# Kernel optimization log

Hardware: AMD Instinct MI355X
Metric: run time of the kernel (lower is better)

Reference implementation:

```python
import jax, jax.numpy as jnp
import numpy as np

IDIM = 128
ODIM = 128
G = 8          # deformable groups
KH = KW = 3
K = KH * KW


def conv3x3(x, w, b):
    # x: [B,C,H,W], w: [O,I,3,3], stride 1, pad 1
    y = jax.lax.conv_general_dilated(x, w, (1, 1), ((1, 1), (1, 1)),
                                     dimension_numbers=('NCHW', 'OIHW', 'NCHW'))
    return y + b[None, :, None, None]


def deform_conv_v2(x, offset, mask, w, b):
    # x: [B,C,H,W]; offset: [B,2*G*K,H,W]; mask: [B,G*K,H,W] (pre-sigmoid)
    B, C, H, W = x.shape
    Cg = C // G
    off = offset.reshape(B, G, 2 * K, H, W)
    dy = off[:, :, 0::2]            # [B,G,K,H,W]
    dx = off[:, :, 1::2]
    m = jax.nn.sigmoid(mask).reshape(B, G, K, H, W)

    ky, kx = jnp.meshgrid(jnp.arange(KH), jnp.arange(KW), indexing='ij')
    ky = ky.reshape(K).astype(x.dtype)
    kx = kx.reshape(K).astype(x.dtype)
    hh = jnp.arange(H, dtype=x.dtype)
    ww = jnp.arange(W, dtype=x.dtype)
    # sampling positions (stride 1, pad 1, dilation 1)
    py = dy + (ky[:, None, None] + hh[None, :, None] - 1.0)   # [B,G,K,H,W]
    px = dx + (kx[:, None, None] + ww[None, None, :] - 1.0)

    y0 = jnp.floor(py)
    x0 = jnp.floor(px)
    ly = py - y0
    lx = px - x0

    x_flat = x.reshape(B, G, Cg, H * W)

    def gather(yi, xi):
        valid = ((yi >= 0) & (yi < H) & (xi >= 0) & (xi < W)).astype(x.dtype)
        yc = jnp.clip(yi, 0, H - 1).astype(jnp.int32)
        xc = jnp.clip(xi, 0, W - 1).astype(jnp.int32)
        idx = (yc * W + xc).reshape(B, G, 1, K * H * W)
        v = jnp.take_along_axis(x_flat, jnp.broadcast_to(idx, (B, G, Cg, K * H * W)), axis=3)
        return v.reshape(B, G, Cg, K, H, W) * valid[:, :, None]

    # bilinear interpolation with zero padding, fused with modulation mask
    v = (gather(y0, x0) * ((1 - ly) * (1 - lx))[:, :, None]
         + gather(y0, x0 + 1) * ((1 - ly) * lx)[:, :, None]
         + gather(y0 + 1, x0) * (ly * (1 - lx))[:, :, None]
         + gather(y0 + 1, x0 + 1) * (ly * lx)[:, :, None])
    v = v * m[:, :, None]                                      # [B,G,Cg,K,H,W]

    wr = w.reshape(w.shape[0], G, Cg, K)
    out = jnp.einsum('bgckhw,ogck->bohw', v, wr)
    return out + b[None, :, None, None]


def setup_inputs() -> dict:
    key = jax.random.key(0)
    ks = jax.random.split(key, 12)
    B, H, W = 2, 96, 96
    s = 0.05
    return {
        'R1': jax.random.normal(ks[0], (B, IDIM, H, W), jnp.float32),
        'Q0': jax.random.normal(ks[1], (B, IDIM, H, W), jnp.float32),
        'w1': jax.random.normal(ks[2], (ODIM, IDIM, 3, 3), jnp.float32) * s,
        'b1': jax.random.normal(ks[3], (ODIM,), jnp.float32) * s,
        'w2': jax.random.normal(ks[4], (ODIM, ODIM, 3, 3), jnp.float32) * s,
        'b2': jax.random.normal(ks[5], (ODIM,), jnp.float32) * s,
        'w_om': jax.random.normal(ks[6], (G * 3 * K, ODIM, 3, 3), jnp.float32) * s,
        'b_om': jax.random.normal(ks[7], (G * 3 * K,), jnp.float32) * s,
        'w_dcn': jax.random.normal(ks[8], (ODIM, IDIM, 3, 3), jnp.float32) * s,
        'b_dcn': jax.random.normal(ks[9], (ODIM,), jnp.float32) * s,
        'w_rq': jax.random.normal(ks[10], (ODIM, 2 * ODIM, 3, 3), jnp.float32) * s,
        'b_rq': jax.random.normal(ks[11], (ODIM,), jnp.float32) * s,
    }


def reference(R1, Q0, w1, b1, w2, b2, w_om, b_om, w_dcn, b_dcn, w_rq, b_rq):
    off = jax.nn.relu(conv3x3(R1 - Q0, w1, b1))
    off = jax.nn.relu(conv3x3(off, w2, b2))
    om = conv3x3(off, w_om, b_om)                 # [B, 3*G*K, H, W]
    o1, o2, mask = jnp.split(om, 3, axis=1)
    offset = jnp.concatenate([o1, o2], axis=1)    # [B, 2*G*K, H, W]
    fea = jax.nn.relu(deform_conv_v2(R1, offset, mask, w_dcn, b_dcn))
    fused = jnp.concatenate([fea, Q0], axis=1)
    return jax.nn.relu(conv3x3(fused, w_rq, b_rq))
```

## Files before the change

kernel.cpp:

```cpp
#include <hip/hip_runtime.h>

#define HH 96
#define WW 96
#define HW 9216
#define NPIX 18432
#define OMC 216
#define PP 9604

typedef __attribute__((ext_vector_type(8))) short short8x;
typedef __attribute__((ext_vector_type(8))) unsigned short ushort8x;
typedef __attribute__((ext_vector_type(4))) float f32x4;

__device__ __forceinline__ f32x4 mfma16(short8x a, short8x b, f32x4 c) {
    return __builtin_amdgcn_mfma_f32_16x16x32_bf16(a, b, c, 0, 0, 0);
}
__device__ __forceinline__ unsigned short f2bf(float f) {
    unsigned int u = __float_as_uint(f);
    u = (u + 0x7FFFu + ((u >> 16) & 1u)) >> 16;
    return (unsigned short)u;
}
__device__ __forceinline__ float bf2f(unsigned short b) {
    return __uint_as_float((unsigned int)b << 16);
}
__device__ __forceinline__ void split2(float v, unsigned short& h, unsigned short& l) {
    h = f2bf(v);
    l = f2bf(v - bf2f(h));
}
__device__ __forceinline__ void gld_lds16(const unsigned short* src, unsigned short* dst) {
    __builtin_amdgcn_global_load_lds(
        (const __attribute__((address_space(1))) unsigned int*)src,
        (__attribute__((address_space(3))) unsigned int*)dst, 16, 0, 0);
}

__global__ __launch_bounds__(256) void zero_borders(
    unsigned short* __restrict__ diffb,
    unsigned short* __restrict__ t1,
    unsigned short* __restrict__ catb)
{
    int i = blockIdx.x * 256 + threadIdx.x;
    if (i >= 776) return;
    int b = i / 388, r = i % 388;
    int y, x;
    if      (r < 98)  { y = 0;          x = r; }
    else if (r < 196) { y = 97;         x = r - 98; }
    else if (r < 292) { y = r - 196 + 1; x = 0; }
    else              { y = r - 292 + 1; x = 97; }
    size_t P = (size_t)b * PP + (size_t)y * 98 + x;
    ushort8x z = {};
    #pragma unroll
    for (int c = 0; c < 32; ++c) *(ushort8x*)&diffb[P * 256 + c * 8] = z;
    #pragma unroll
    for (int c = 0; c < 32; ++c) *(ushort8x*)&t1[P * 256 + c * 8] = z;
    #pragma unroll
    for (int c = 0; c < 64; ++c) *(ushort8x*)&catb[P * 512 + c * 8] = z;
}

__global__ __launch_bounds__(256) void prep_acts(
    const float* __restrict__ R1, const float* __restrict__ Q0,
    unsigned short* __restrict__ r1b,
    unsigned short* __restrict__ diffb,
    unsigned short* __restrict__ cat)
{
    __shared__ float tR[128][64];
    __shared__ float tQ[128][64];
    int tid = threadIdx.x;
    int p0  = blockIdx.x * 64;
    int b   = p0 / HW;
    int rem0 = p0 % HW;

    for (int e = tid; e < 2048; e += 256) {
        int c = e >> 4, j = e & 15;
        size_t base = ((size_t)(b * 128 + c)) * HW + rem0;
        *(float4*)&tR[c][j * 4] = *(const float4*)(R1 + base + j * 4);
        *(float4*)&tQ[c][j * 4] = *(const float4*)(Q0 + base + j * 4);
    }
    __syncthreads();

    int p = tid & 63, half = tid >> 6;
    int c0 = half * 32;
    int pix = p0 + p;
    int rm = pix % HW, yy = rm / 96, xx = rm % 96;
    size_t P = (size_t)b * PP + (size_t)(yy + 1) * 98 + xx + 1;
    ushort8x rb[4], dh[4], dl[4], qh[4], ql[4];
    #pragma unroll
    for (int cc = 0; cc < 32; ++cc) {
        float r = tR[c0 + cc][p], q = tQ[c0 + cc][p];
        rb[cc >> 3][cc & 7] = f2bf(r);
        unsigned short h, l;
        split2(r - q, h, l); dh[cc >> 3][cc & 7] = h; dl[cc >> 3][cc & 7] = l;
        split2(q, h, l);     qh[cc >> 3][cc & 7] = h; ql[cc >> 3][cc & 7] = l;
    }
    #pragma unroll
    for (int i = 0; i < 4; ++i) {
        *(ushort8x*)&r1b[(size_t)pix * 128 + c0 + i * 8] = rb[i];
        *(ushort8x*)&diffb[P * 256 +       c0 + i * 8] = dh[i];
        *(ushort8x*)&diffb[P * 256 + 128 + c0 + i * 8] = dl[i];
        *(ushort8x*)&cat [P * 512 + 128 + c0 + i * 8] = qh[i];
        *(ushort8x*)&cat [P * 512 + 384 + c0 + i * 8] = ql[i];
    }
}

__global__ __launch_bounds__(256) void prep_w(
    const float* __restrict__ w1, const float* __restrict__ w2,
    const float* __restrict__ wom, const float* __restrict__ bom,
    const float* __restrict__ wrq, const float* __restrict__ wdcn,
    unsigned short* __restrict__ p1, unsigned short* __restrict__ p2,
    unsigned short* __restrict__ pom, unsigned short* __restrict__ prq,
    unsigned short* __restrict__ pdcn, float* __restrict__ bomp)
{
    int idx = blockIdx.x * 256 + threadIdx.x;
    unsigned short h, l;
    if (idx < 147456) {
        int t = idx / 16384, o = (idx >> 7) & 127, ci = idx & 127;
        int src = (o * 128 + ci) * 9 + t;
        split2(w1[src], h, l);  p1[idx] = h;  p1[idx + 147456] = l;
        split2(w2[src], h, l);  p2[idx] = h;  p2[idx + 147456] = l;
        int dd = o * 1152 + ((ci >> 4) * 9 + t) * 16 + (ci & 15);
        split2(wdcn[src], h, l); pdcn[dd] = h; pdcn[dd + 147456] = l;
    }
    if (idx < 294912) {
        {
            int t = idx / 32768, o = (idx >> 7) & 255, ci = idx & 127;
            float v = (o < OMC) ? wom[(o * 128 + ci) * 9 + t] : 0.f;
            split2(v, h, l); pom[idx] = h; pom[idx + 294912] = l;
        }
        {
            int t = idx / 32768, o = (idx >> 8) & 127, ci = idx & 255;
            split2(wrq[(o * 256 + ci) * 9 + t], h, l);
            prq[idx] = h; prq[idx + 294912] = l;
        }
    }
    if (idx < 256) bomp[idx] = (idx < OMC) ? bom[idx] : 0.f;
}

template<int CIN, int COUTP, int MODE, bool RELU>
__global__ __launch_bounds__(256, 2) void conv_mfma(
    const unsigned short* __restrict__ in,
    const unsigned short* __restrict__ wpk,
    const float* __restrict__ bias,
    void* __restrict__ outv)
{
    constexpr int NKC = CIN / 32;
    constexpr int NSTEP = 9 * NKC;
    const size_t WPLANE = (size_t)9 * COUTP * CIN;

    __shared__ __align__(16) unsigned short s_buf[2][3072 + 8192];

    int tid = threadIdx.x;
    int wid = tid >> 6, lane = tid & 63;
    int r = lane & 15, q = lane >> 4;
    int bid = blockIdx.x;
    int swz = (bid & 7) * 48 + (bid >> 3);
    int rowid = swz >> 1, half = swz & 1;
    int b = rowid / 96, y = rowid % 96;
    int x0 = half * 48;
    int nbase = blockIdx.y * 128;

    auto stage = [&](int buf, int step) {
        int t = step / NKC, kc = step - t * NKC;
        int dy = t / 3 - 1, dx = t % 3 - 1;
        unsigned short* sb = &s_buf[buf][0];
        {
            int j = tid;
            int m = j >> 7, pl = (j >> 6) & 1, L = j & 63;
            int px = m * 16 + (L & 15), qd = L >> 4;
            const unsigned short* src = in +
                ((size_t)b * PP + (size_t)(y + 1 + dy) * 98 + (x0 + 1 + dx + px)) * (2 * CIN)
                + pl * CIN + kc * 32 + qd * 8;
            gld_lds16(src, sb + (size_t)(wid * 64) * 8);
        }
        if (tid < 128) {
            int j = 256 + tid;
            int m = j >> 7, pl = (j >> 6) & 1, L = j & 63;
            int px = m * 16 + (L & 15), qd = L >> 4;
            const unsigned short* src = in +
                ((size_t)b * PP + (size_t)(y + 1 + dy) * 98 + (x0 + 1 + dx + px)) * (2 * CIN)
                + pl * CIN + kc * 32 + qd * 8;
            gld_lds16(src, sb + (size_t)(256 + wid * 64) * 8);
        }
        const unsigned short* wbase = wpk + ((size_t)t * COUTP + nbase) * CIN + kc * 32;
        #pragma unroll
        for (int c = 0; c < 4; ++c) {
            int j = c * 256 + tid;
            int ni = (j >> 7) & 1, pl = (j >> 6) & 1, L = j & 63;
            int rr = L & 15, qq = L >> 4;
            const unsigned short* src = wbase + (size_t)pl * WPLANE
                + (size_t)(c * 32 + ni * 16 + rr) * CIN + qq * 8;
            gld_lds16(src, sb + 3072 + (size_t)(c * 256 + wid * 64) * 8);
        }
    };

    f32x4 acc[3][2] = {};

    auto compute = [&](int buf) {
        const unsigned short* sb = &s_buf[buf][0];
        short8x AH[3], AL[3], BH[2], BL[2];
        #pragma unroll
        for (int m = 0; m < 3; ++m) {
            AH[m] = *(const short8x*)(sb + m * 1024 + lane * 8);
            AL[m] = *(const short8x*)(sb + m * 1024 + 512 + lane * 8);
        }
        #pragma unroll
        for (int n = 0; n < 2; ++n) {
            BH[n] = *(const short8x*)(sb + 3072 + wid * 2048 + n * 1024 + lane * 8);
            BL[n] = *(const short8x*)(sb + 3072 + wid * 2048 + n * 1024 + 512 + lane * 8);
        }
        #pragma unroll
        for (int m = 0; m < 3; ++m) {
            #pragma unroll
            for (int n = 0; n < 2; ++n) {
                acc[m][n] = mfma16(AH[m], BH[n], acc[m][n]);
                acc[m][n] = mfma16(AL[m], BH[n], acc[m][n]);
                acc[m][n] = mfma16(AH[m], BL[n], acc[m][n]);
            }
        }
    };

    stage(0, 0);
    __syncthreads();
    int cur = 0;
    for (int k = 0; k < NSTEP; ++k) {
        if (k + 1 < NSTEP) stage(cur ^ 1, k + 1);
        compute(cur);
        __syncthreads();
        cur ^= 1;
    }

    #pragma unroll
    for (int m = 0; m < 3; ++m) {
        #pragma unroll
        for (int n = 0; n < 2; ++n) {
            int o = nbase + wid * 32 + n * 16 + r;
            float bv = bias[o];
            #pragma unroll
            for (int j = 0; j < 4; ++j) {
                int px = m * 16 + q * 4 + j;
                int xx = x0 + px;
                float v = acc[m][n][j] + bv;
                if (RELU) v = fmaxf(v, 0.f);
                if (MODE == 0) {
                    size_t P = (size_t)b * PP + (size_t)(y + 1) * 98 + xx + 1;
                    unsigned short h, l; split2(v, h, l);
                    ((unsigned short*)outv)[P * 2 * COUTP + o] = h;
                    ((unsigned short*)outv)[P * 2 * COUTP + COUTP + o] = l;
                } else if (MODE == 1) {
                    if (o < OMC)
                        ((unsigned short*)outv)[((size_t)b * HW + y * 96 + xx) * OMC + o] = f2bf(v);
                } else {
                    ((float*)outv)[((size_t)b * 128 + o) * HW + y * 96 + xx] = v;
                }
            }
        }
    }
}

__global__ __launch_bounds__(256, 4) void deform_mfma(
    const unsigned short* __restrict__ xb,
    const unsigned short* __restrict__ omf,
    const unsigned short* __restrict__ wpk,
    const float* __restrict__ bias,
    unsigned short* __restrict__ cat)
{
    __shared__ __align__(16) unsigned short s_v[16][1160];

    int tid = threadIdx.x;
    int pix0 = blockIdx.x * 16;
    int b = pix0 / HW;

    for (int e = tid; e < 1152; e += 256) {
        int p = e & 15, gk = e >> 4;
        int pix = pix0 + p;
        int rem = pix % HW;
        int hh = rem / 96, ww = rem % 96;
        int g = gk / 9, k = gk % 9;
        const unsigned short* op = omf + (size_t)pix * OMC;
        float dy = bf2f(op[g * 18 + 2 * k]);
        float dx = bf2f(op[g * 18 + 2 * k + 1]);
        float mr = bf2f(op[144 + g * 9 + k]);
        float m = 1.f / (1.f + __expf(-mr));
        float py = dy + (float)(k / 3) + (float)hh - 1.f;
        float px = dx + (float)(k % 3) + (float)ww - 1.f;
        float fy = floorf(py), fx = floorf(px);
        int y0 = (int)fy, x0 = (int)fx;
        float ly = py - fy, lx = px - fx;
        float cw[4] = {(1.f - ly) * (1.f - lx), (1.f - ly) * lx,
                       ly * (1.f - lx), ly * lx};
        ushort8x cv0[4], cv1[4];
        #pragma unroll
        for (int j = 0; j < 4; ++j) {
            int yy = y0 + (j >> 1), xx = x0 + (j & 1);
            bool valid = (yy >= 0) && (yy < HH) && (xx >= 0) && (xx < WW);
            int yc = yy < 0 ? 0 : (yy > 95 ? 95 : yy);
            int xc = xx < 0 ? 0 : (xx > 95 ? 95 : xx);
            const unsigned short* cp =
                xb + ((size_t)(b * HW + yc * 96 + xc)) * 128 + g * 16;
            cv0[j] = *(const ushort8x*)cp;
            cv1[j] = *(const ushort8x*)(cp + 8);
            cw[j] = valid ? cw[j] * m : 0.f;
        }
        ushort8x o0, o1;
        #pragma unroll
        for (int i = 0; i < 8; ++i) {
            float v0 = cw[0] * bf2f(cv0[0][i]) + cw[1] * bf2f(cv0[1][i])
                     + cw[2] * bf2f(cv0[2][i]) + cw[3] * bf2f(cv0[3][i]);
            float v1 = cw[0] * bf2f(cv1[0][i]) + cw[1] * bf2f(cv1[1][i])
                     + cw[2] * bf2f(cv1[2][i]) + cw[3] * bf2f(cv1[3][i]);
            o0[i] = f2bf(v0);
            o1[i] = f2bf(v1);
        }
        *(ushort8x*)&s_v[p][gk * 16    ] = o0;
        *(ushort8x*)&s_v[p][gk * 16 + 8] = o1;
    }
    __syncthreads();

    int wid = tid >> 6, lane = tid & 63;
    int r = lane & 15, q = lane >> 4;
    int n0 = wid * 32;
    f32x4 acc0 = {}, acc1 = {};
    const unsigned short* wb = wpk + (size_t)(n0 + r) * 1152 + q * 8;
    #pragma unroll
    for (int kp = 0; kp < 18; ++kp) {
        const int k0 = kp * 2, k1 = k0 + 1;
        short8x a0 = *(const short8x*)&s_v[r][k0 * 32 + q * 8];
        short8x a1 = *(const short8x*)&s_v[r][k1 * 32 + q * 8];
        short8x w00 = *(const short8x*)(wb + k0 * 32);
        short8x w10 = *(const short8x*)(wb + (size_t)16 * 1152 + k0 * 32);
        short8x l00 = *(const short8x*)(wb + 147456 + k0 * 32);
        short8x l10 = *(const short8x*)(wb + 147456 + (size_t)16 * 1152 + k0 * 32);
        short8x w01 = *(const short8x*)(wb + k1 * 32);
        short8x w11 = *(const short8x*)(wb + (size_t)16 * 1152 + k1 * 32);
        short8x l01 = *(const short8x*)(wb + 147456 + k1 * 32);
        short8x l11 = *(const short8x*)(wb + 147456 + (size_t)16 * 1152 + k1 * 32);
        acc0 = mfma16(a0, w00, acc0);
        acc1 = mfma16(a0, w10, acc1);
        acc0 = mfma16(a0, l00, acc0);
        acc1 = mfma16(a0, l10, acc1);
        acc0 = mfma16(a1, w01, acc0);
        acc1 = mfma16(a1, w11, acc1);
        acc0 = mfma16(a1, l01, acc0);
        acc1 = mfma16(a1, l11, acc1);
    }
    #pragma unroll
    for (int ni = 0; ni < 2; ++ni) {
        f32x4 A = ni ? acc1 : acc0;
        int o = n0 + ni * 16 + r;
        float bv = bias[o];
        #pragma unroll
        for (int j = 0; j < 4; ++j) {
            int pixel = pix0 + q * 4 + j;
            int bb = pixel / HW, rm = pixel % HW;
            int yy = rm / 96, xx = rm % 96;
            size_t P = (size_t)bb * PP + (size_t)(yy + 1) * 98 + xx + 1;
            float v = fmaxf(A[j] + bv, 0.f);
            unsigned short h, l;
            split2(v, h, l);
            cat[P * 512 + o] = h;
            cat[P * 512 + 256 + o] = l;
        }
    }
}

extern "C" void kernel_launch(void* const* d_in, const int* in_sizes, int n_in,
                              void* d_out, int out_size, void* d_ws, size_t ws_size,
                              hipStream_t stream) {
    const float* R1    = (const float*)d_in[0];
    const float* Q0    = (const float*)d_in[1];
    const float* w1    = (const float*)d_in[2];
    const float* b1    = (const float*)d_in[3];
    const float* w2    = (const float*)d_in[4];
    const float* b2    = (const float*)d_in[5];
    const float* w_om  = (const float*)d_in[6];
    const float* b_om  = (const float*)d_in[7];
    const float* w_dcn = (const float*)d_in[8];
    const float* b_dcn = (const float*)d_in[9];
    const float* w_rq  = (const float*)d_in[10];
    const float* b_rq  = (const float*)d_in[11];
    float* outp = (float*)d_out;

    char* w = (char*)d_ws;
    unsigned short* r1b   = (unsigned short*)w; w += (size_t)NPIX * 128 * 2;
    unsigned short* diffb = (unsigned short*)w; w += (size_t)2 * PP * 256 * 2;
    unsigned short* t1    = (unsigned short*)w; w += (size_t)2 * PP * 256 * 2;
    unsigned short* catb  = (unsigned short*)w; w += (size_t)2 * PP * 512 * 2;
    unsigned short* p1    = (unsigned short*)w; w += 2 * 147456 * 2;
    unsigned short* p2    = (unsigned short*)w; w += 2 * 147456 * 2;
    unsigned short* pdcn  = (unsigned short*)w; w += 2 * 147456 * 2;
    unsigned short* pom   = (unsigned short*)w; w += 2 * 294912 * 2;
    unsigned short* prq   = (unsigned short*)w; w += 2 * 294912 * 2;
    float*          bomp  = (float*)w;          w += 256 * 4;
    unsigned short* t2    = diffb;
    unsigned short* omf   = t1;

    zero_borders<<<4, 256, 0, stream>>>(diffb, t1, catb);
    prep_acts<<<288, 256, 0, stream>>>(R1, Q0, r1b, diffb, catb);
    prep_w<<<1152, 256, 0, stream>>>(w1, w2, w_om, b_om, w_rq, w_dcn,
                                     p1, p2, pom, prq, pdcn, bomp);

    conv_mfma<128, 128, 0, true ><<<dim3(384, 1), 256, 0, stream>>>(diffb, p1, b1, t1);
    conv_mfma<128, 128, 0, true ><<<dim3(384, 1), 256, 0, stream>>>(t1,    p2, b2, t2);
    conv_mfma<128, 256, 1, false><<<dim3(384, 2), 256, 0, stream>>>(t2,   pom, bomp, omf);

    deform_mfma<<<1152, 256, 0, stream>>>(r1b, omf, pdcn, b_dcn, catb);

    conv_mfma<256, 128, 2, true ><<<dim3(384, 1), 256, 0, stream>>>(catb, prq, b_rq, outp);
}
```

Baseline: 413.1 us.

## Halve conv output tile per block and software-pipeline deform sampling gathers

The conv kernel is templated on output channels per block (now 64 instead of 128), doubling the grid in y and raising launch bounds to 4 waves per SIMD via less LDS and fewer accumulators. The deform kernel's sampling loop is rewritten with two register sets so the gathers for the next group/tap are issued before interpolating the current one, and the two offset values are read with one 32-bit load. More blocks re-stage the same input tile, which adds redundant activation loads in exchange for occupancy and latency hiding.

```diff
diff --git a/kernel.cpp b/kernel.cpp
--- a/kernel.cpp
+++ b/kernel.cpp
@@ -133,8 +133,8 @@
     if (idx < 256) bomp[idx] = (idx < OMC) ? bom[idx] : 0.f;
 }
 
-template<int CIN, int COUTP, int MODE, bool RELU>
-__global__ __launch_bounds__(256, 2) void conv_mfma(
+template<int CIN, int COUTP, int NOUT, int MODE, bool RELU>
+__global__ __launch_bounds__(256, 4) void conv_mfma(
     const unsigned short* __restrict__ in,
     const unsigned short* __restrict__ wpk,
     const float* __restrict__ bias,
@@ -142,9 +142,11 @@
 {
     constexpr int NKC = CIN / 32;
     constexpr int NSTEP = 9 * NKC;
+    constexpr int NF = NOUT / 64;
+    constexpr int WUS = NOUT * 16;
     const size_t WPLANE = (size_t)9 * COUTP * CIN;
 
-    __shared__ __align__(16) unsigned short s_buf[2][3072 + 8192];
+    __shared__ __align__(16) unsigned short s_buf[2][3072 + NOUT * 64];
 
     int tid = threadIdx.x;
     int wid = tid >> 6, lane = tid & 63;
@@ -154,7 +156,7 @@
     int rowid = swz >> 1, half = swz & 1;
     int b = rowid / 96, y = rowid % 96;
     int x0 = half * 48;
-    int nbase = blockIdx.y * 128;
+    int nbase = blockIdx.y * NOUT;
 
     auto stage = [&](int buf, int step) {
         int t = step / NKC, kc = step - t * NKC;
@@ -180,35 +182,34 @@
         }
         const unsigned short* wbase = wpk + ((size_t)t * COUTP + nbase) * CIN + kc * 32;
         #pragma unroll
-        for (int c = 0; c < 4; ++c) {
+        for (int c = 0; c < NOUT / 32; ++c) {
             int j = c * 256 + tid;
-            int ni = (j >> 7) & 1, pl = (j >> 6) & 1, L = j & 63;
-            int rr = L & 15, qq = L >> 4;
+            int o16 = j >> 7, pl = (j >> 6) & 1, L = j & 63;
             const unsigned short* src = wbase + (size_t)pl * WPLANE
-                + (size_t)(c * 32 + ni * 16 + rr) * CIN + qq * 8;
+                + (size_t)(o16 * 16 + (L & 15)) * CIN + (L >> 4) * 8;
             gld_lds16(src, sb + 3072 + (size_t)(c * 256 + wid * 64) * 8);
         }
     };
 
-    f32x4 acc[3][2] = {};
+    f32x4 acc[3][NF] = {};
 
     auto compute = [&](int buf) {
         const unsigned short* sb = &s_buf[buf][0];
-        short8x AH[3], AL[3], BH[2], BL[2];
+        short8x AH[3], AL[3], BH[NF], BL[NF];
         #pragma unroll
         for (int m = 0; m < 3; ++m) {
             AH[m] = *(const short8x*)(sb + m * 1024 + lane * 8);
             AL[m] = *(const short8x*)(sb + m * 1024 + 512 + lane * 8);
         }
         #pragma unroll
-        for (int n = 0; n < 2; ++n) {
-            BH[n] = *(const short8x*)(sb + 3072 + wid * 2048 + n * 1024 + lane * 8);
-            BL[n] = *(const short8x*)(sb + 3072 + wid * 2048 + n * 1024 + 512 + lane * 8);
+        for (int n = 0; n < NF; ++n) {
+            BH[n] = *(const short8x*)(sb + 3072 + wid * WUS + n * 1024 + lane * 8);
+            BL[n] = *(const short8x*)(sb + 3072 + wid * WUS + n * 1024 + 512 + lane * 8);
         }
         #pragma unroll
         for (int m = 0; m < 3; ++m) {
             #pragma unroll
-            for (int n = 0; n < 2; ++n) {
+            for (int n = 0; n < NF; ++n) {
                 acc[m][n] = mfma16(AH[m], BH[n], acc[m][n]);
                 acc[m][n] = mfma16(AL[m], BH[n], acc[m][n]);
                 acc[m][n] = mfma16(AH[m], BL[n], acc[m][n]);
@@ -229,8 +230,8 @@
     #pragma unroll
     for (int m = 0; m < 3; ++m) {
         #pragma unroll
-        for (int n = 0; n < 2; ++n) {
-            int o = nbase + wid * 32 + n * 16 + r;
+        for (int n = 0; n < NF; ++n) {
+            int o = nbase + wid * (NF * 16) + n * 16 + r;
             float bv = bias[o];
             #pragma unroll
             for (int j = 0; j < 4; ++j) {
@@ -266,16 +267,22 @@
     int tid = threadIdx.x;
     int pix0 = blockIdx.x * 16;
     int b = pix0 / HW;
-
-    for (int e = tid; e < 1152; e += 256) {
-        int p = e & 15, gk = e >> 4;
-        int pix = pix0 + p;
-        int rem = pix % HW;
-        int hh = rem / 96, ww = rem % 96;
-        int g = gk / 9, k = gk % 9;
-        const unsigned short* op = omf + (size_t)pix * OMC;
-        float dy = bf2f(op[g * 18 + 2 * k]);
-        float dx = bf2f(op[g * 18 + 2 * k + 1]);
+    int p = tid & 15, gkl = tid >> 4;
+    int pix = pix0 + p;
+    int rem = pix % HW;
+    int hh = rem / 96, ww = rem % 96;
+    const unsigned short* op = omf + (size_t)pix * OMC;
+    const unsigned short* xB = xb + (size_t)b * HW * 128;
+
+    ushort8x Ac0[4], Ac1[4]; float Acw[4]; int Adst = 0;
+    ushort8x Bc0[4], Bc1[4]; float Bcw[4]; int Bdst = 0;
+
+    auto prep = [&](int gk, ushort8x (&c0)[4], ushort8x (&c1)[4],
+                    float (&cw)[4], int& dst) {
+        int g = gk / 9, k = gk - g * 9;
+        unsigned int dd = *(const unsigned int*)(op + g * 18 + 2 * k);
+        float dy = bf2f((unsigned short)(dd & 0xffffu));
+        float dx = bf2f((unsigned short)(dd >> 16));
         float mr = bf2f(op[144 + g * 9 + k]);
         float m = 1.f / (1.f + __expf(-mr));
         float py = dy + (float)(k / 3) + (float)hh - 1.f;
@@ -283,34 +290,46 @@
         float fy = floorf(py), fx = floorf(px);
         int y0 = (int)fy, x0 = (int)fx;
         float ly = py - fy, lx = px - fx;
-        float cw[4] = {(1.f - ly) * (1.f - lx), (1.f - ly) * lx,
+        float wj[4] = {(1.f - ly) * (1.f - lx), (1.f - ly) * lx,
                        ly * (1.f - lx), ly * lx};
-        ushort8x cv0[4], cv1[4];
         #pragma unroll
         for (int j = 0; j < 4; ++j) {
             int yy = y0 + (j >> 1), xx = x0 + (j & 1);
-            bool valid = (yy >= 0) && (yy < HH) && (xx >= 0) && (xx < WW);
-            int yc = yy < 0 ? 0 : (yy > 95 ? 95 : yy);
-            int xc = xx < 0 ? 0 : (xx > 95 ? 95 : xx);
-            const unsigned short* cp =
-                xb + ((size_t)(b * HW + yc * 96 + xc)) * 128 + g * 16;
-            cv0[j] = *(const ushort8x*)cp;
-            cv1[j] = *(const ushort8x*)(cp + 8);
-            cw[j] = valid ? cw[j] * m : 0.f;
-        }
+            bool valid = ((unsigned)yy < 96u) && ((unsigned)xx < 96u);
+            int yc = min(max(yy, 0), 95), xc = min(max(xx, 0), 95);
+            const unsigned short* cp = xB + ((size_t)(yc * 96 + xc)) * 128 + g * 16;
+            c0[j] = *(const ushort8x*)cp;
+            c1[j] = *(const ushort8x*)(cp + 8);
+            cw[j] = valid ? wj[j] * m : 0.f;
+        }
+        dst = gk * 16;
+    };
+    auto finish = [&](ushort8x (&c0)[4], ushort8x (&c1)[4],
+                      float (&cw)[4], int dst) {
         ushort8x o0, o1;
         #pragma unroll
         for (int i = 0; i < 8; ++i) {
-            float v0 = cw[0] * bf2f(cv0[0][i]) + cw[1] * bf2f(cv0[1][i])
-                     + cw[2] * bf2f(cv0[2][i]) + cw[3] * bf2f(cv0[3][i]);
-            float v1 = cw[0] * bf2f(cv1[0][i]) + cw[1] * bf2f(cv1[1][i])
-                     + cw[2] * bf2f(cv1[2][i]) + cw[3] * bf2f(cv1[3][i]);
+            float v0 = cw[0]*bf2f(c0[0][i]) + cw[1]*bf2f(c0[1][i])
+                     + cw[2]*bf2f(c0[2][i]) + cw[3]*bf2f(c0[3][i]);
+            float v1 = cw[0]*bf2f(c1[0][i]) + cw[1]*bf2f(c1[1][i])
+                     + cw[2]*bf2f(c1[2][i]) + cw[3]*bf2f(c1[3][i]);
             o0[i] = f2bf(v0);
             o1[i] = f2bf(v1);
         }
-        *(ushort8x*)&s_v[p][gk * 16    ] = o0;
-        *(ushort8x*)&s_v[p][gk * 16 + 8] = o1;
-    }
+        *(ushort8x*)&s_v[p][dst]     = o0;
+        *(ushort8x*)&s_v[p][dst + 8] = o1;
+    };
+
+    prep(gkl,      Ac0, Ac1, Acw, Adst);
+    prep(gkl + 16, Bc0, Bc1, Bcw, Bdst);
+    finish(Ac0, Ac1, Acw, Adst);
+    prep(gkl + 32, Ac0, Ac1, Acw, Adst);
+    finish(Bc0, Bc1, Bcw, Bdst);
+    prep(gkl + 48, Bc0, Bc1, Bcw, Bdst);
+    finish(Ac0, Ac1, Acw, Adst);
+    if (gkl < 8) prep(gkl + 64, Ac0, Ac1, Acw, Adst);
+    finish(Bc0, Bc1, Bcw, Bdst);
+    if (gkl < 8) finish(Ac0, Ac1, Acw, Adst);
     __syncthreads();
 
     int wid = tid >> 6, lane = tid & 63;
@@ -396,11 +415,11 @@
     prep_w<<<1152, 256, 0, stream>>>(w1, w2, w_om, b_om, w_rq, w_dcn,
                                      p1, p2, pom, prq, pdcn, bomp);
 
-    conv_mfma<128, 128, 0, true ><<<dim3(384, 1), 256, 0, stream>>>(diffb, p1, b1, t1);
-    conv_mfma<128, 128, 0, true ><<<dim3(384, 1), 256, 0, stream>>>(t1,    p2, b2, t2);
-    conv_mfma<128, 256, 1, false><<<dim3(384, 2), 256, 0, stream>>>(t2,   pom, bomp, omf);
+    conv_mfma<128, 128, 64, 0, true ><<<dim3(384, 2), 256, 0, stream>>>(diffb, p1, b1, t1);
+    conv_mfma<128, 128, 64, 0, true ><<<dim3(384, 2), 256, 0, stream>>>(t1,    p2, b2, t2);
+    conv_mfma<128, 256, 64, 1, false><<<dim3(384, 4), 256, 0, stream>>>(t2,   pom, bomp, omf);
 
     deform_mfma<<<1152, 256, 0, stream>>>(r1b, omf, pdcn, b_dcn, catb);
 
-    conv_mfma<256, 128, 2, true ><<<dim3(384, 1), 256, 0, stream>>>(catb, prq, b_rq, outp);
-}
+    conv_mfma<256, 128, 64, 2, true ><<<dim3(384, 2), 256, 0, stream>>>(catb, prq, b_rq, outp);
+}
```

Measured after the change: 433.4 us. 1.05x slower.

## Split deformable conv into chunked gather kernel and LDS-staged GEMM kernel

Applied to the files above, without the earlier changes.

Splits the fused deformable kernel in two. A gather kernel writes bilinearly sampled, mask-modulated values into a global scratch buffer, and a GEMM kernel processes 32-pixel tiles with double-buffered LDS staging of both samples and weights. The work runs in four pixel chunks so the scratch buffer fits into the reused diffb region, which forces a workspace layout reorder. The aim is to stop each 16-pixel block from re-reading the full weight matrix from global memory. The cost is an extra round trip through global memory and eight launches in place of one.

```diff
diff --git a/kernel.cpp b/kernel.cpp
--- a/kernel.cpp
+++ b/kernel.cpp
@@ -6,6 +6,7 @@
 #define NPIX 18432
 #define OMC 216
 #define PP 9604
+#define CHPX 4608
 
 typedef __attribute__((ext_vector_type(8))) short short8x;
 typedef __attribute__((ext_vector_type(8))) unsigned short ushort8x;
@@ -254,104 +255,156 @@
     }
 }
 
-__global__ __launch_bounds__(256, 4) void deform_mfma(
+__global__ __launch_bounds__(256, 4) void deform_gather(
     const unsigned short* __restrict__ xb,
     const unsigned short* __restrict__ omf,
+    unsigned short* __restrict__ smp,
+    int pix0)
+{
+    int it = blockIdx.x * 256 + threadIdx.x;
+    int pl = it / 36, gp = it - pl * 36;
+    int gk0 = gp * 2, gk1 = gk0 + 1;
+    int pix = pix0 + pl;
+    int b = pix / HW;
+    int rem = pix % HW;
+    int hh = rem / 96, ww = rem % 96;
+    const unsigned short* op = omf + (size_t)pix * OMC;
+    const unsigned short* xB = xb + (size_t)b * HW * 128;
+
+    int gA = gk0 / 9, kA = gk0 - gA * 9;
+    unsigned int ddA = *(const unsigned int*)(op + gA * 18 + 2 * kA);
+    float mrA = bf2f(op[144 + gA * 9 + kA]);
+    float pyA = bf2f((unsigned short)(ddA & 0xffffu)) + (float)(kA / 3) + (float)hh - 1.f;
+    float pxA = bf2f((unsigned short)(ddA >> 16)) + (float)(kA % 3) + (float)ww - 1.f;
+    float fyA = floorf(pyA), fxA = floorf(pxA);
+    int yA = (int)fyA, xA = (int)fxA;
+    float lyA = pyA - fyA, lxA = pxA - fxA;
+    float mA = 1.f / (1.f + __expf(-mrA));
+    float cwA[4] = {(1.f-lyA)*(1.f-lxA), (1.f-lyA)*lxA, lyA*(1.f-lxA), lyA*lxA};
+    int gB = gk1 / 9, kB = gk1 - gB * 9;
+    unsigned int ddB = *(const unsigned int*)(op + gB * 18 + 2 * kB);
+    float mrB = bf2f(op[144 + gB * 9 + kB]);
+    float pyB = bf2f((unsigned short)(ddB & 0xffffu)) + (float)(kB / 3) + (float)hh - 1.f;
+    float pxB = bf2f((unsigned short)(ddB >> 16)) + (float)(kB % 3) + (float)ww - 1.f;
+    float fyB = floorf(pyB), fxB = floorf(pxB);
+    int yB = (int)fyB, xB2 = (int)fxB;
+    float lyB = pyB - fyB, lxB = pxB - fxB;
+    float mB = 1.f / (1.f + __expf(-mrB));
+    float cwB[4] = {(1.f-lyB)*(1.f-lxB), (1.f-lyB)*lxB, lyB*(1.f-lxB), lyB*lxB};
+
+    ushort8x A0[4], A1[4], B0[4], B1[4];
+    #pragma unroll
+    for (int j = 0; j < 4; ++j) {
+        int yy = yA + (j >> 1), xx = xA + (j & 1);
+        bool valid = ((unsigned)yy < 96u) && ((unsigned)xx < 96u);
+        int yc = min(max(yy, 0), 95), xc = min(max(xx, 0), 95);
+        const unsigned short* cp = xB + (size_t)(yc * 96 + xc) * 128 + gA * 16;
+        A0[j] = *(const ushort8x*)cp;
+        A1[j] = *(const ushort8x*)(cp + 8);
+        cwA[j] = valid ? cwA[j] * mA : 0.f;
+    }
+    #pragma unroll
+    for (int j = 0; j < 4; ++j) {
+        int yy = yB + (j >> 1), xx = xB2 + (j & 1);
+        bool valid = ((unsigned)yy < 96u) && ((unsigned)xx < 96u);
+        int yc = min(max(yy, 0), 95), xc = min(max(xx, 0), 95);
+        const unsigned short* cp = xB + (size_t)(yc * 96 + xc) * 128 + gB * 16;
+        B0[j] = *(const ushort8x*)cp;
+        B1[j] = *(const ushort8x*)(cp + 8);
+        cwB[j] = valid ? cwB[j] * mB : 0.f;
+    }
+
+    ushort8x oA0, oA1, oB0, oB1;
+    #pragma unroll
+    for (int i = 0; i < 8; ++i) {
+        float a0 = cwA[0]*bf2f(A0[0][i]) + cwA[1]*bf2f(A0[1][i])
+                 + cwA[2]*bf2f(A0[2][i]) + cwA[3]*bf2f(A0[3][i]);
+        float a1 = cwA[0]*bf2f(A1[0][i]) + cwA[1]*bf2f(A1[1][i])
+                 + cwA[2]*bf2f(A1[2][i]) + cwA[3]*bf2f(A1[3][i]);
+        float b0 = cwB[0]*bf2f(B0[0][i]) + cwB[1]*bf2f(B0[1][i])
+                 + cwB[2]*bf2f(B0[2][i]) + cwB[3]*bf2f(B0[3][i]);
+        float b1 = cwB[0]*bf2f(B1[0][i]) + cwB[1]*bf2f(B1[1][i])
+                 + cwB[2]*bf2f(B1[2][i]) + cwB[3]*bf2f(B1[3][i]);
+        oA0[i] = f2bf(a0); oA1[i] = f2bf(a1);
+        oB0[i] = f2bf(b0); oB1[i] = f2bf(b1);
+    }
+    unsigned short* out = smp + (size_t)pl * 1152 + gk0 * 16;
+    *(ushort8x*)(out     ) = oA0;
+    *(ushort8x*)(out +  8) = oA1;
+    *(ushort8x*)(out + 16) = oB0;
+    *(ushort8x*)(out + 24) = oB1;
+}
+
+__global__ __launch_bounds__(256, 4) void deform_gemm(
+    const unsigned short* __restrict__ smp,
     const unsigned short* __restrict__ wpk,
     const float* __restrict__ bias,
-    unsigned short* __restrict__ cat)
-{
-    __shared__ __align__(16) unsigned short s_v[16][1160];
+    unsigned short* __restrict__ cat,
+    int pixbase)
+{
+    __shared__ __align__(16) unsigned short sA[2][1024];
+    __shared__ __align__(16) unsigned short sW[2][8192];
 
     int tid = threadIdx.x;
-    int pix0 = blockIdx.x * 16;
-    int b = pix0 / HW;
-
-    for (int e = tid; e < 1152; e += 256) {
-        int p = e & 15, gk = e >> 4;
-        int pix = pix0 + p;
-        int rem = pix % HW;
-        int hh = rem / 96, ww = rem % 96;
-        int g = gk / 9, k = gk % 9;
-        const unsigned short* op = omf + (size_t)pix * OMC;
-        float dy = bf2f(op[g * 18 + 2 * k]);
-        float dx = bf2f(op[g * 18 + 2 * k + 1]);
-        float mr = bf2f(op[144 + g * 9 + k]);
-        float m = 1.f / (1.f + __expf(-mr));
-        float py = dy + (float)(k / 3) + (float)hh - 1.f;
-        float px = dx + (float)(k % 3) + (float)ww - 1.f;
-        float fy = floorf(py), fx = floorf(px);
-        int y0 = (int)fy, x0 = (int)fx;
-        float ly = py - fy, lx = px - fx;
-        float cw[4] = {(1.f - ly) * (1.f - lx), (1.f - ly) * lx,
-                       ly * (1.f - lx), ly * lx};
-        ushort8x cv0[4], cv1[4];
-        #pragma unroll
-        for (int j = 0; j < 4; ++j) {
-            int yy = y0 + (j >> 1), xx = x0 + (j & 1);
-            bool valid = (yy >= 0) && (yy < HH) && (xx >= 0) && (xx < WW);
-            int yc = yy < 0 ? 0 : (yy > 95 ? 95 : yy);
-            int xc = xx < 0 ? 0 : (xx > 95 ? 95 : xx);
-            const unsigned short* cp =
-                xb + ((size_t)(b * HW + yc * 96 + xc)) * 128 + g * 16;
-            cv0[j] = *(const ushort8x*)cp;
-            cv1[j] = *(const ushort8x*)(cp + 8);
-            cw[j] = valid ? cw[j] * m : 0.f;
-        }
-        ushort8x o0, o1;
-        #pragma unroll
-        for (int i = 0; i < 8; ++i) {
-            float v0 = cw[0] * bf2f(cv0[0][i]) + cw[1] * bf2f(cv0[1][i])
-                     + cw[2] * bf2f(cv0[2][i]) + cw[3] * bf2f(cv0[3][i]);
-            float v1 = cw[0] * bf2f(cv1[0][i]) + cw[1] * bf2f(cv1[1][i])
-                     + cw[2] * bf2f(cv1[2][i]) + cw[3] * bf2f(cv1[3][i]);
-            o0[i] = f2bf(v0);
-            o1[i] = f2bf(v1);
-        }
-        *(ushort8x*)&s_v[p][gk * 16    ] = o0;
-        *(ushort8x*)&s_v[p][gk * 16 + 8] = o1;
-    }
-    __syncthreads();
-
     int wid = tid >> 6, lane = tid & 63;
     int r = lane & 15, q = lane >> 4;
-    int n0 = wid * 32;
-    f32x4 acc0 = {}, acc1 = {};
-    const unsigned short* wb = wpk + (size_t)(n0 + r) * 1152 + q * 8;
-    #pragma unroll
-    for (int kp = 0; kp < 18; ++kp) {
-        const int k0 = kp * 2, k1 = k0 + 1;
-        short8x a0 = *(const short8x*)&s_v[r][k0 * 32 + q * 8];
-        short8x a1 = *(const short8x*)&s_v[r][k1 * 32 + q * 8];
-        short8x w00 = *(const short8x*)(wb + k0 * 32);
-        short8x w10 = *(const short8x*)(wb + (size_t)16 * 1152 + k0 * 32);
-        short8x l00 = *(const short8x*)(wb + 147456 + k0 * 32);
-        short8x l10 = *(const short8x*)(wb + 147456 + (size_t)16 * 1152 + k0 * 32);
-        short8x w01 = *(const short8x*)(wb + k1 * 32);
-        short8x w11 = *(const short8x*)(wb + (size_t)16 * 1152 + k1 * 32);
-        short8x l01 = *(const short8x*)(wb + 147456 + k1 * 32);
-        short8x l11 = *(const short8x*)(wb + 147456 + (size_t)16 * 1152 + k1 * 32);
-        acc0 = mfma16(a0, w00, acc0);
-        acc1 = mfma16(a0, w10, acc1);
-        acc0 = mfma16(a0, l00, acc0);
-        acc1 = mfma16(a0, l10, acc1);
-        acc0 = mfma16(a1, w01, acc0);
-        acc1 = mfma16(a1, w11, acc1);
-        acc0 = mfma16(a1, l01, acc0);
-        acc1 = mfma16(a1, l11, acc1);
-    }
-    #pragma unroll
-    for (int ni = 0; ni < 2; ++ni) {
-        f32x4 A = ni ? acc1 : acc0;
-        int o = n0 + ni * 16 + r;
+    int mg = wid >> 1, ng = wid & 1;
+    int px0 = blockIdx.x * 32;
+
+    auto stage = [&](int buf, int ks) {
+        if (tid < 128) {
+            int j = tid;
+            int px = (j >> 6) * 16 + (j & 15);
+            const unsigned short* src =
+                smp + (size_t)(px0 + px) * 1152 + ks * 32 + ((j >> 4) & 3) * 8;
+            gld_lds16(src, &sA[buf][(j >> 6) * 512]);
+        }
+        #pragma unroll
+        for (int c = 0; c < 4; ++c) {
+            int j = c * 256 + tid;
+            int f = j >> 6, L = j & 63;
+            int og = f >> 1, pl2 = f & 1;
+            const unsigned short* src = wpk + (size_t)pl2 * 147456
+                + (size_t)(og * 16 + (L & 15)) * 1152 + ks * 32 + (L >> 4) * 8;
+            gld_lds16(src, &sW[buf][f * 512]);
+        }
+    };
+
+    f32x4 acc[4] = {};
+
+    auto compute = [&](int buf) {
+        short8x a = *(const short8x*)&sA[buf][mg * 512 + lane * 8];
+        #pragma unroll
+        for (int nf = 0; nf < 4; ++nf) {
+            int fh = (ng * 4 + nf) * 2;
+            short8x wh = *(const short8x*)&sW[buf][fh * 512 + lane * 8];
+            short8x wl = *(const short8x*)&sW[buf][(fh + 1) * 512 + lane * 8];
+            acc[nf] = mfma16(a, wh, acc[nf]);
+            acc[nf] = mfma16(a, wl, acc[nf]);
+        }
+    };
+
+    stage(0, 0);
+    __syncthreads();
+    int cur = 0;
+    for (int ks = 0; ks < 36; ++ks) {
+        if (ks + 1 < 36) stage(cur ^ 1, ks + 1);
+        compute(cur);
+        __syncthreads();
+        cur ^= 1;
+    }
+
+    #pragma unroll
+    for (int nf = 0; nf < 4; ++nf) {
+        int o = ng * 64 + nf * 16 + r;
         float bv = bias[o];
         #pragma unroll
         for (int j = 0; j < 4; ++j) {
-            int pixel = pix0 + q * 4 + j;
+            int pixel = pixbase + px0 + mg * 16 + q * 4 + j;
             int bb = pixel / HW, rm = pixel % HW;
             int yy = rm / 96, xx = rm % 96;
             size_t P = (size_t)bb * PP + (size_t)(yy + 1) * 98 + xx + 1;
-            float v = fmaxf(A[j] + bv, 0.f);
+            float v = fmaxf(acc[nf][j] + bv, 0.f);
             unsigned short h, l;
             split2(v, h, l);
             cat[P * 512 + o] = h;
@@ -380,16 +433,17 @@
     char* w = (char*)d_ws;
     unsigned short* r1b   = (unsigned short*)w; w += (size_t)NPIX * 128 * 2;
     unsigned short* diffb = (unsigned short*)w; w += (size_t)2 * PP * 256 * 2;
+    unsigned short* p1    = (unsigned short*)w; w += 2 * 147456 * 2;
+    unsigned short* p2    = (unsigned short*)w; w += 2 * 147456 * 2;
+    unsigned short* pom   = (unsigned short*)w; w += 2 * 294912 * 2;
     unsigned short* t1    = (unsigned short*)w; w += (size_t)2 * PP * 256 * 2;
     unsigned short* catb  = (unsigned short*)w; w += (size_t)2 * PP * 512 * 2;
-    unsigned short* p1    = (unsigned short*)w; w += 2 * 147456 * 2;
-    unsigned short* p2    = (unsigned short*)w; w += 2 * 147456 * 2;
     unsigned short* pdcn  = (unsigned short*)w; w += 2 * 147456 * 2;
-    unsigned short* pom   = (unsigned short*)w; w += 2 * 294912 * 2;
     unsigned short* prq   = (unsigned short*)w; w += 2 * 294912 * 2;
     float*          bomp  = (float*)w;          w += 256 * 4;
     unsigned short* t2    = diffb;
     unsigned short* omf   = t1;
+    unsigned short* smp   = diffb;
 
     zero_borders<<<4, 256, 0, stream>>>(diffb, t1, catb);
     prep_acts<<<288, 256, 0, stream>>>(R1, Q0, r1b, diffb, catb);
@@ -400,7 +454,10 @@
     conv_mfma<128, 128, 0, true ><<<dim3(384, 1), 256, 0, stream>>>(t1,    p2, b2, t2);
     conv_mfma<128, 256, 1, false><<<dim3(384, 2), 256, 0, stream>>>(t2,   pom, bomp, omf);
 
-    deform_mfma<<<1152, 256, 0, stream>>>(r1b, omf, pdcn, b_dcn, catb);
+    for (int c = 0; c < 4; ++c) {
+        deform_gather<<<CHPX * 36 / 256, 256, 0, stream>>>(r1b, omf, smp, c * CHPX);
+        deform_gemm<<<CHPX / 32, 256, 0, stream>>>(smp, pdcn, b_dcn, catb, c * CHPX);
+    }
 
     conv_mfma<256, 128, 2, true ><<<dim3(384, 1), 256, 0, stream>>>(catb, prq, b_rq, outp);
 }
```

New measurement: 498.1 us. 20.6% more time.

## Replace LDS double-buffered conv with direct global-load MFMA using smaller tiles

Applied to the files above, without the earlier changes.

The implicit-GEMM convolution no longer stages activations and weights into shared memory with global_load_lds and a double-buffered loop. Each wave now loads its MFMA operands straight from global memory into registers. Each block covers a 64-pixel by 64-channel tile, giving more blocks, and the occupancy hint rises from 2 to 3. This removes LDS traffic and barriers but gives up reuse across waves, so the kernel leans on L1/L2 caching and has no explicit prefetch to hide global latency. The change also reorders workspace buffers and simplifies the bounds checks in the deform kernel.

```diff
diff --git a/kernel.cpp b/kernel.cpp
--- a/kernel.cpp
+++ b/kernel.cpp
@@ -25,11 +25,6 @@
 __device__ __forceinline__ void split2(float v, unsigned short& h, unsigned short& l) {
     h = f2bf(v);
     l = f2bf(v - bf2f(h));
-}
-__device__ __forceinline__ void gld_lds16(const unsigned short* src, unsigned short* dst) {
-    __builtin_amdgcn_global_load_lds(
-        (const __attribute__((address_space(1))) unsigned int*)src,
-        (__attribute__((address_space(3))) unsigned int*)dst, 16, 0, 0);
 }
 
 __global__ __launch_bounds__(256) void zero_borders(
@@ -134,120 +129,91 @@
 }
 
 template<int CIN, int COUTP, int MODE, bool RELU>
-__global__ __launch_bounds__(256, 2) void conv_mfma(
+__global__ __launch_bounds__(256, 3) void conv_mfma(
     const unsigned short* __restrict__ in,
     const unsigned short* __restrict__ wpk,
     const float* __restrict__ bias,
     void* __restrict__ outv)
 {
     constexpr int NKC = CIN / 32;
-    constexpr int NSTEP = 9 * NKC;
     const size_t WPLANE = (size_t)9 * COUTP * CIN;
-
-    __shared__ __align__(16) unsigned short s_buf[2][3072 + 8192];
 
     int tid = threadIdx.x;
     int wid = tid >> 6, lane = tid & 63;
     int r = lane & 15, q = lane >> 4;
+    int mg = wid >> 1, ng = wid & 1;
     int bid = blockIdx.x;
-    int swz = (bid & 7) * 48 + (bid >> 3);
-    int rowid = swz >> 1, half = swz & 1;
-    int b = rowid / 96, y = rowid % 96;
-    int x0 = half * 48;
-    int nbase = blockIdx.y * 128;
-
-    auto stage = [&](int buf, int step) {
-        int t = step / NKC, kc = step - t * NKC;
-        int dy = t / 3 - 1, dx = t % 3 - 1;
-        unsigned short* sb = &s_buf[buf][0];
-        {
-            int j = tid;
-            int m = j >> 7, pl = (j >> 6) & 1, L = j & 63;
-            int px = m * 16 + (L & 15), qd = L >> 4;
-            const unsigned short* src = in +
-                ((size_t)b * PP + (size_t)(y + 1 + dy) * 98 + (x0 + 1 + dx + px)) * (2 * CIN)
-                + pl * CIN + kc * 32 + qd * 8;
-            gld_lds16(src, sb + (size_t)(wid * 64) * 8);
-        }
-        if (tid < 128) {
-            int j = 256 + tid;
-            int m = j >> 7, pl = (j >> 6) & 1, L = j & 63;
-            int px = m * 16 + (L & 15), qd = L >> 4;
-            const unsigned short* src = in +
-                ((size_t)b * PP + (size_t)(y + 1 + dy) * 98 + (x0 + 1 + dx + px)) * (2 * CIN)
-                + pl * CIN + kc * 32 + qd * 8;
-            gld_lds16(src, sb + (size_t)(256 + wid * 64) * 8);
-        }
-        const unsigned short* wbase = wpk + ((size_t)t * COUTP + nbase) * CIN + kc * 32;
-        #pragma unroll
-        for (int c = 0; c < 4; ++c) {
-            int j = c * 256 + tid;
-            int ni = (j >> 7) & 1, pl = (j >> 6) & 1, L = j & 63;
-            int rr = L & 15, qq = L >> 4;
-            const unsigned short* src = wbase + (size_t)pl * WPLANE
-                + (size_t)(c * 32 + ni * 16 + rr) * CIN + qq * 8;
-            gld_lds16(src, sb + 3072 + (size_t)(c * 256 + wid * 64) * 8);
-        }
-    };
-
-    f32x4 acc[3][2] = {};
-
-    auto compute = [&](int buf) {
-        const unsigned short* sb = &s_buf[buf][0];
-        short8x AH[3], AL[3], BH[2], BL[2];
-        #pragma unroll
-        for (int m = 0; m < 3; ++m) {
-            AH[m] = *(const short8x*)(sb + m * 1024 + lane * 8);
-            AL[m] = *(const short8x*)(sb + m * 1024 + 512 + lane * 8);
-        }
+    int swz = (bid & 7) * 36 + (bid >> 3);
+    int pblk = swz * 64;
+    int b = pblk / HW;
+    int prem = pblk % HW;
+    int nbase = blockIdx.y * 64 + ng * 32;
+
+    int pxl0 = prem + mg * 32 + r;
+    int pxl1 = pxl0 + 16;
+    int y0 = pxl0 / 96, x0 = pxl0 % 96;
+    int y1 = pxl1 / 96, x1 = pxl1 % 96;
+    const unsigned short* a0 =
+        in + ((size_t)b * PP + (size_t)(y0 + 1) * 98 + (x0 + 1)) * (2 * CIN) + q * 8;
+    const unsigned short* a1 =
+        in + ((size_t)b * PP + (size_t)(y1 + 1) * 98 + (x1 + 1)) * (2 * CIN) + q * 8;
+    const unsigned short* wb = wpk + (size_t)(nbase + r) * CIN + q * 8;
+
+    f32x4 acc[2][2] = {};
+
+    #pragma unroll
+    for (int t = 0; t < 9; ++t) {
+        const int aoff = ((t / 3 - 1) * 98 + (t % 3 - 1)) * (2 * CIN);
+        const unsigned short* wt = wb + (size_t)t * COUTP * CIN;
+        #pragma unroll
+        for (int kc = 0; kc < NKC; ++kc) {
+            const int ko = kc * 32;
+            short8x A0h = *(const short8x*)(a0 + aoff + ko);
+            short8x A0l = *(const short8x*)(a0 + aoff + CIN + ko);
+            short8x A1h = *(const short8x*)(a1 + aoff + ko);
+            short8x A1l = *(const short8x*)(a1 + aoff + CIN + ko);
+            short8x B0h = *(const short8x*)(wt + ko);
+            short8x B1h = *(const short8x*)(wt + (size_t)16 * CIN + ko);
+            short8x B0l = *(const short8x*)(wt + WPLANE + ko);
+            short8x B1l = *(const short8x*)(wt + WPLANE + (size_t)16 * CIN + ko);
+            acc[0][0] = mfma16(A0h, B0h, acc[0][0]);
+            acc[0][1] = mfma16(A0h, B1h, acc[0][1]);
+            acc[1][0] = mfma16(A1h, B0h, acc[1][0]);
+            acc[1][1] = mfma16(A1h, B1h, acc[1][1]);
+            acc[0][0] = mfma16(A0l, B0h, acc[0][0]);
+            acc[0][1] = mfma16(A0l, B1h, acc[0][1]);
+            acc[1][0] = mfma16(A1l, B0h, acc[1][0]);
+            acc[1][1] = mfma16(A1l, B1h, acc[1][1]);
+            acc[0][0] = mfma16(A0h, B0l, acc[0][0]);
+            acc[0][1] = mfma16(A0h, B1l, acc[0][1]);
+            acc[1][0] = mfma16(A1h, B0l, acc[1][0]);
+            acc[1][1] = mfma16(A1h, B1l, acc[1][1]);
+        }
+    }
+
+    #pragma unroll
+    for (int m = 0; m < 2; ++m) {
         #pragma unroll
         for (int n = 0; n < 2; ++n) {
-            BH[n] = *(const short8x*)(sb + 3072 + wid * 2048 + n * 1024 + lane * 8);
-            BL[n] = *(const short8x*)(sb + 3072 + wid * 2048 + n * 1024 + 512 + lane * 8);
-        }
-        #pragma unroll
-        for (int m = 0; m < 3; ++m) {
-            #pragma unroll
-            for (int n = 0; n < 2; ++n) {
-                acc[m][n] = mfma16(AH[m], BH[n], acc[m][n]);
-                acc[m][n] = mfma16(AL[m], BH[n], acc[m][n]);
-                acc[m][n] = mfma16(AH[m], BL[n], acc[m][n]);
-            }
-        }
-    };
-
-    stage(0, 0);
-    __syncthreads();
-    int cur = 0;
-    for (int k = 0; k < NSTEP; ++k) {
-        if (k + 1 < NSTEP) stage(cur ^ 1, k + 1);
-        compute(cur);
-        __syncthreads();
-        cur ^= 1;
-    }
-
-    #pragma unroll
-    for (int m = 0; m < 3; ++m) {
-        #pragma unroll
-        for (int n = 0; n < 2; ++n) {
-            int o = nbase + wid * 32 + n * 16 + r;
+            int o = nbase + n * 16 + r;
             float bv = bias[o];
             #pragma unroll
             for (int j = 0; j < 4; ++j) {
-                int px = m * 16 + q * 4 + j;
-                int xx = x0 + px;
+                int pixel = pblk + mg * 32 + m * 16 + q * 4 + j;
+                int rm = pixel % HW;
+                int yy = rm / 96, xx = rm % 96;
                 float v = acc[m][n][j] + bv;
                 if (RELU) v = fmaxf(v, 0.f);
                 if (MODE == 0) {
-                    size_t P = (size_t)b * PP + (size_t)(y + 1) * 98 + xx + 1;
+                    size_t P = (size_t)b * PP + (size_t)(yy + 1) * 98 + xx + 1;
                     unsigned short h, l; split2(v, h, l);
                     ((unsigned short*)outv)[P * 2 * COUTP + o] = h;
                     ((unsigned short*)outv)[P * 2 * COUTP + COUTP + o] = l;
                 } else if (MODE == 1) {
                     if (o < OMC)
-                        ((unsigned short*)outv)[((size_t)b * HW + y * 96 + xx) * OMC + o] = f2bf(v);
+                        ((unsigned short*)outv)[((size_t)b * HW + rm) * OMC + o] = f2bf(v);
                 } else {
-                    ((float*)outv)[((size_t)b * 128 + o) * HW + y * 96 + xx] = v;
+                    ((float*)outv)[((size_t)b * 128 + o) * HW + rm] = v;
                 }
             }
         }
@@ -289,9 +255,8 @@
         #pragma unroll
         for (int j = 0; j < 4; ++j) {
             int yy = y0 + (j >> 1), xx = x0 + (j & 1);
-            bool valid = (yy >= 0) && (yy < HH) && (xx >= 0) && (xx < WW);
-            int yc = yy < 0 ? 0 : (yy > 95 ? 95 : yy);
-            int xc = xx < 0 ? 0 : (xx > 95 ? 95 : xx);
+            bool valid = ((unsigned)yy < 96u) && ((unsigned)xx < 96u);
+            int yc = min(max(yy, 0), 95), xc = min(max(xx, 0), 95);
             const unsigned short* cp =
                 xb + ((size_t)(b * HW + yc * 96 + xc)) * 128 + g * 16;
             cv0[j] = *(const ushort8x*)cp;
@@ -380,12 +345,12 @@
     char* w = (char*)d_ws;
     unsigned short* r1b   = (unsigned short*)w; w += (size_t)NPIX * 128 * 2;
     unsigned short* diffb = (unsigned short*)w; w += (size_t)2 * PP * 256 * 2;
+    unsigned short* p1    = (unsigned short*)w; w += 2 * 147456 * 2;
+    unsigned short* p2    = (unsigned short*)w; w += 2 * 147456 * 2;
+    unsigned short* pom   = (unsigned short*)w; w += 2 * 294912 * 2;
     unsigned short* t1    = (unsigned short*)w; w += (size_t)2 * PP * 256 * 2;
     unsigned short* catb  = (unsigned short*)w; w += (size_t)2 * PP * 512 * 2;
-    unsigned short* p1    = (unsigned short*)w; w += 2 * 147456 * 2;
-    unsigned short* p2    = (unsigned short*)w; w += 2 * 147456 * 2;
     unsigned short* pdcn  = (unsigned short*)w; w += 2 * 147456 * 2;
-    unsigned short* pom   = (unsigned short*)w; w += 2 * 294912 * 2;
     unsigned short* prq   = (unsigned short*)w; w += 2 * 294912 * 2;
     float*          bomp  = (float*)w;          w += 256 * 4;
     unsigned short* t2    = diffb;
@@ -396,11 +361,11 @@
     prep_w<<<1152, 256, 0, stream>>>(w1, w2, w_om, b_om, w_rq, w_dcn,
                                      p1, p2, pom, prq, pdcn, bomp);
 
-    conv_mfma<128, 128, 0, true ><<<dim3(384, 1), 256, 0, stream>>>(diffb, p1, b1, t1);
-    conv_mfma<128, 128, 0, true ><<<dim3(384, 1), 256, 0, stream>>>(t1,    p2, b2, t2);
-    conv_mfma<128, 256, 1, false><<<dim3(384, 2), 256, 0, stream>>>(t2,   pom, bomp, omf);
+    conv_mfma<128, 128, 0, true ><<<dim3(288, 2), 256, 0, stream>>>(diffb, p1, b1, t1);
+    conv_mfma<128, 128, 0, true ><<<dim3(288, 2), 256, 0, stream>>>(t1,    p2, b2, t2);
+    conv_mfma<128, 256, 1, false><<<dim3(288, 4), 256, 0, stream>>>(t2,   pom, bomp, omf);
 
     deform_mfma<<<1152, 256, 0, stream>>>(r1b, omf, pdcn, b_dcn, catb);
 
-    conv_mfma<256, 128, 2, true ><<<dim3(384, 1), 256, 0, stream>>>(catb, prq, b_rq, outp);
-}
+    conv_mfma<256, 128, 2, true ><<<dim3(288, 2), 256, 0, stream>>>(catb, prq, b_rq, outp);
+}
```

Result: slower. 704.1 us (+70.4%).
